# Kernel optimization log

Hardware: AMD Instinct MI355X
Metric: run time of the kernel (lower is better)

Reference implementation:

```python
import jax, jax.numpy as jnp
import numpy as np

# Module hyperparameters (match init_kwargs)
RES_SCALE = 1.0
INPUT_SCALE = 1.0
LEAK = 0.9  # leak_rate
SEQ_LEN = 4096
INPUT_SIZE = 128
RES_SIZE = 2048
BIAS_SCALE = 0.4


def setup_inputs() -> dict:
    key = jax.random.key(0)
    k1, k2, k3, k4 = jax.random.split(key, 4)
    return {
        "input_data": jax.random.normal(k1, (SEQ_LEN, INPUT_SIZE), jnp.float32),
        "W_in": jax.random.normal(k2, (RES_SIZE, INPUT_SIZE), jnp.float32),
        "W_res": jax.random.normal(k3, (RES_SIZE, RES_SIZE), jnp.float32),
        "bias": BIAS_SCALE * jax.random.normal(k4, (RES_SIZE,), jnp.float32),
    }


def reference(input_data, W_in, W_res, bias):
    """ESN forward with f=erf, random_projection='gpu', no initial_state.

    x[i] = (1-leak)*x[i-1]
           + leak * erf(res_scale*W_res@x[i-1] + input_scale*W_in@u[i] + bias) / sqrt(res_size)
    Returns states of shape (seq_len, res_size).
    """
    res_size = W_res.shape[0]
    inv_sqrt = jnp.asarray(1.0 / np.sqrt(res_size), input_data.dtype)
    # Batch the input projection into one GEMM: (T, res)
    proj_in = INPUT_SCALE * input_data @ W_in.T + bias

    def step(s, u_t):
        pre = RES_SCALE * (W_res @ s) + u_t
        s_new = (1.0 - LEAK) * s + LEAK * jax.lax.erf(pre) * inv_sqrt
        return s_new, s_new

    s0 = jnp.zeros((res_size,), input_data.dtype)
    _, xs = jax.lax.scan(step, s0, proj_in)
    return xs
```

## Files before the change

kernel.cpp:

```cpp
#include <hip/hip_runtime.h>
#include <hip/hip_cooperative_groups.h>
#include <math.h>

typedef unsigned int u32x4 __attribute__((ext_vector_type(4)));
typedef unsigned long long ull;

constexpr int T = 4096;
constexpr int R = 2048;
constexpr int J = 128;
constexpr float ONE_MINUS_LEAK = 0.1f;
constexpr float LEAK = 0.9f;
constexpr float INV_SQRT_R = 0.022097086912079608f;

constexpr int NWG  = 64;
constexpr int NREP = 2;

__global__ __launch_bounds__(256) void esn_proj_kernel(
    const float* __restrict__ U, const float* __restrict__ Win,
    const float* __restrict__ bias, float* __restrict__ out)
{
    __shared__ float As[16][129];
    __shared__ float Bs[16][129];
    const int tb = blockIdx.x * 16;
    const int rb = blockIdx.y * 16;
    const int tid = threadIdx.x;

    for (int i = tid; i < 16 * J; i += 256) {
        int r = i >> 7, c = i & 127;
        As[r][c] = U[(size_t)(tb + r) * J + c];
        Bs[r][c] = Win[(size_t)(rb + r) * J + c];
    }
    __syncthreads();

    const int ti = tid >> 4;
    const int rj = tid & 15;
    float acc = 0.f;
#pragma unroll
    for (int k = 0; k < J; ++k) acc = fmaf(As[ti][k], Bs[rj][k], acc);
    out[(size_t)(tb + ti) * R + (rb + rj)] = acc + bias[rb + rj];
}

__global__ __launch_bounds__(512) void esn_recur_kernel(
    const float* __restrict__ Wres, float* __restrict__ out,
    ull* __restrict__ slots )
{
    const int wg   = blockIdx.x;
    const int tid  = threadIdx.x;
    const int wv   = tid >> 6;
    const int lane = tid & 63;
    const int rowbase = wg * 32 + wv * 4;
    const int rep  = wg & (NREP - 1);

    float w[4][32];
#pragma unroll
    for (int j = 0; j < 4; ++j) {
        const float* wr = Wres + (size_t)(rowbase + j) * R + lane;
#pragma unroll
        for (int k = 0; k < 32; ++k) w[j][k] = wr[k * 64];
    }

    __shared__ __align__(16) float xs[2][R];
    float xold = 0.f;
    long  spin = 0;

    for (int t = 0; t < T; ++t) {
        float proj = (lane < 4) ? out[(size_t)t * R + rowbase + lane] : 0.f;

        const ull* src = slots + ((size_t)((t & 1) * NREP + rep)) * R;
        const ull* p0 = src + 2 * tid;
        const ull* p1 = src + 1024 + 2 * tid;
        const unsigned want = (unsigned)t;
        u32x4 v0, v1;
        while (true) {
            asm volatile(
                "global_load_dwordx4 %0, %2, off sc0 sc1\n\t"
                "global_load_dwordx4 %1, %3, off sc0 sc1\n\t"
                "s_waitcnt vmcnt(0)"
                : "=&v"(v0), "=&v"(v1)
                : "v"(p0), "v"(p1)
                : "memory");
            if (v0[1] == want && v0[3] == want &&
                v1[1] == want && v1[3] == want) break;
            if (++spin > (1L << 26)) break;
        }
        float* xb = xs[t & 1];
        xb[2 * tid]        = __uint_as_float(v0[0]);
        xb[2 * tid + 1]    = __uint_as_float(v0[2]);
        xb[2 * tid + 1024] = __uint_as_float(v1[0]);
        xb[2 * tid + 1025] = __uint_as_float(v1[2]);
        __syncthreads();

        const float* x = xs[t & 1];
        float xr[32];
#pragma unroll
        for (int k = 0; k < 32; ++k) xr[k] = x[k * 64 + lane];

        float mysum = 0.f;
#pragma unroll
        for (int j = 0; j < 4; ++j) {
            float a0 = 0.f, a1 = 0.f, a2 = 0.f, a3 = 0.f;
#pragma unroll
            for (int k = 0; k < 8; ++k) {
                a0 = fmaf(w[j][4 * k + 0], xr[4 * k + 0], a0);
                a1 = fmaf(w[j][4 * k + 1], xr[4 * k + 1], a1);
                a2 = fmaf(w[j][4 * k + 2], xr[4 * k + 2], a2);
                a3 = fmaf(w[j][4 * k + 3], xr[4 * k + 3], a3);
            }
            float acc = (a0 + a1) + (a2 + a3);
#pragma unroll
            for (int off = 32; off > 0; off >>= 1)
                acc += __shfl_xor(acc, off);
            if (lane == j) mysum = acc;
        }

        if (lane < 4) {
            const float pre  = mysum + proj;
            const float xnew = ONE_MINUS_LEAK * xold +
                               LEAK * erff(pre) * INV_SQRT_R;
            xold = xnew;
            const ull packed = ((ull)(unsigned)(t + 1) << 32) |
                               (ull)__float_as_uint(xnew);
            const size_t pb = (size_t)(((t + 1) & 1) * NREP) * R
                            + rowbase + lane;
#pragma unroll
            for (int g = 0; g < NREP; ++g)
                __hip_atomic_store(&slots[pb + (size_t)g * R], packed,
                                   __ATOMIC_RELAXED, __HIP_MEMORY_SCOPE_AGENT);
            out[(size_t)t * R + rowbase + lane] = xnew;
        }
    }
}

extern "C" void kernel_launch(void* const* d_in, const int* in_sizes, int n_in,
                              void* d_out, int out_size, void* d_ws, size_t ws_size,
                              hipStream_t stream) {
    const float* U    = (const float*)d_in[0];
    const float* Win  = (const float*)d_in[1];
    const float* Wres = (const float*)d_in[2];
    const float* bias = (const float*)d_in[3];
    float* out = (float*)d_out;
    ull* slots = (ull*)d_ws;

    hipMemsetAsync(slots, 0, (size_t)2 * NREP * R * sizeof(ull), stream);

    dim3 pgrid(T / 16, R / 16);
    esn_proj_kernel<<<pgrid, dim3(256), 0, stream>>>(U, Win, bias, out);

    void* args[] = { (void*)&Wres, (void*)&out, (void*)&slots };
    hipLaunchCooperativeKernel((const void*)esn_recur_kernel,
                               dim3(NWG), dim3(512), args, 0, stream);
}
```

Baseline: 11.39 ms.

## Double recurrence workgroup threads to 1024 with two rows per wave

Each recurrence workgroup now runs 1024 threads (16 waves), and each wave owns 2 reservoir rows instead of 4. The per-thread register footprint for W_res halves, each thread polls one 16-byte slot chunk instead of two, and the reduction interleaves two shuffle chains. The aim is to shorten the per-step critical path (polling, FMA and reduction) by spreading the work over more waves. The trade-off is heavier barrier synchronisation across 16 waves and possibly lower per-wave throughput.

```diff
diff --git a/kernel.cpp b/kernel.cpp
--- a/kernel.cpp
+++ b/kernel.cpp
@@ -40,7 +40,7 @@
     out[(size_t)(tb + ti) * R + (rb + rj)] = acc + bias[rb + rj];
 }
 
-__global__ __launch_bounds__(512) void esn_recur_kernel(
+__global__ __launch_bounds__(1024) void esn_recur_kernel(
     const float* __restrict__ Wres, float* __restrict__ out,
     ull* __restrict__ slots )
 {
@@ -48,15 +48,15 @@
     const int tid  = threadIdx.x;
     const int wv   = tid >> 6;
     const int lane = tid & 63;
-    const int rowbase = wg * 32 + wv * 4;
+    const int rowbase = wg * 32 + wv * 2;
     const int rep  = wg & (NREP - 1);
 
-    float w[4][32];
+    float w0[32], w1[32];
+    {
+        const float* wr0 = Wres + (size_t)(rowbase + 0) * R + lane;
+        const float* wr1 = Wres + (size_t)(rowbase + 1) * R + lane;
 #pragma unroll
-    for (int j = 0; j < 4; ++j) {
-        const float* wr = Wres + (size_t)(rowbase + j) * R + lane;
-#pragma unroll
-        for (int k = 0; k < 32; ++k) w[j][k] = wr[k * 64];
+        for (int k = 0; k < 32; ++k) { w0[k] = wr0[k * 64]; w1[k] = wr1[k * 64]; }
     }
 
     __shared__ __align__(16) float xs[2][R];
@@ -64,56 +64,46 @@
     long  spin = 0;
 
     for (int t = 0; t < T; ++t) {
-        float proj = (lane < 4) ? out[(size_t)t * R + rowbase + lane] : 0.f;
+        float proj = (lane < 2) ? out[(size_t)t * R + rowbase + lane] : 0.f;
 
         const ull* src = slots + ((size_t)((t & 1) * NREP + rep)) * R;
         const ull* p0 = src + 2 * tid;
-        const ull* p1 = src + 1024 + 2 * tid;
         const unsigned want = (unsigned)t;
-        u32x4 v0, v1;
+        u32x4 v0;
         while (true) {
             asm volatile(
-                "global_load_dwordx4 %0, %2, off sc0 sc1\n\t"
-                "global_load_dwordx4 %1, %3, off sc0 sc1\n\t"
+                "global_load_dwordx4 %0, %1, off sc0 sc1\n\t"
                 "s_waitcnt vmcnt(0)"
-                : "=&v"(v0), "=&v"(v1)
-                : "v"(p0), "v"(p1)
-                : "memory");
-            if (v0[1] == want && v0[3] == want &&
-                v1[1] == want && v1[3] == want) break;
+                : "=&v"(v0) : "v"(p0) : "memory");
+            if (v0[1] == want && v0[3] == want) break;
             if (++spin > (1L << 26)) break;
         }
         float* xb = xs[t & 1];
-        xb[2 * tid]        = __uint_as_float(v0[0]);
-        xb[2 * tid + 1]    = __uint_as_float(v0[2]);
-        xb[2 * tid + 1024] = __uint_as_float(v1[0]);
-        xb[2 * tid + 1025] = __uint_as_float(v1[2]);
+        *(float2*)&xb[2 * tid] = make_float2(__uint_as_float(v0[0]),
+                                            __uint_as_float(v0[2]));
         __syncthreads();
 
         const float* x = xs[t & 1];
-        float xr[32];
+        float a0 = 0.f, a1 = 0.f, b0 = 0.f, b1 = 0.f;
 #pragma unroll
-        for (int k = 0; k < 32; ++k) xr[k] = x[k * 64 + lane];
+        for (int k = 0; k < 16; ++k) {
+            const float xk0 = x[(2 * k + 0) * 64 + lane];
+            const float xk1 = x[(2 * k + 1) * 64 + lane];
+            a0 = fmaf(w0[2 * k + 0], xk0, a0);
+            a1 = fmaf(w0[2 * k + 1], xk1, a1);
+            b0 = fmaf(w1[2 * k + 0], xk0, b0);
+            b1 = fmaf(w1[2 * k + 1], xk1, b1);
+        }
+        float accA = a0 + a1;
+        float accB = b0 + b1;
+#pragma unroll
+        for (int off = 32; off > 0; off >>= 1) {
+            accA += __shfl_xor(accA, off);
+            accB += __shfl_xor(accB, off);
+        }
+        const float mysum = (lane == 0) ? accA : accB;
 
-        float mysum = 0.f;
-#pragma unroll
-        for (int j = 0; j < 4; ++j) {
-            float a0 = 0.f, a1 = 0.f, a2 = 0.f, a3 = 0.f;
-#pragma unroll
-            for (int k = 0; k < 8; ++k) {
-                a0 = fmaf(w[j][4 * k + 0], xr[4 * k + 0], a0);
-                a1 = fmaf(w[j][4 * k + 1], xr[4 * k + 1], a1);
-                a2 = fmaf(w[j][4 * k + 2], xr[4 * k + 2], a2);
-                a3 = fmaf(w[j][4 * k + 3], xr[4 * k + 3], a3);
-            }
-            float acc = (a0 + a1) + (a2 + a3);
-#pragma unroll
-            for (int off = 32; off > 0; off >>= 1)
-                acc += __shfl_xor(acc, off);
-            if (lane == j) mysum = acc;
-        }
-
-        if (lane < 4) {
+        if (lane < 2) {
             const float pre  = mysum + proj;
             const float xnew = ONE_MINUS_LEAK * xold +
                                LEAK * erff(pre) * INV_SQRT_R;
@@ -148,5 +138,5 @@
 
     void* args[] = { (void*)&Wres, (void*)&out, (void*)&slots };
     hipLaunchCooperativeKernel((const void*)esn_recur_kernel,
-                               dim3(NWG), dim3(512), args, 0, stream);
+                               dim3(NWG), dim3(1024), args, 0, stream);
 }
```

Result: slower. 14.72 ms (+29.3%).
